# Optimization experiments

Measured on AMD Instinct MI355X. Metric: run time of the kernel, lower is better.

The kernel has to match this reference:

```python
import jax, jax.numpy as jnp
import numpy as np

B, T, E, H, V = 64, 256, 300, 512, 50000
G = 3 * H  # gates: r, z, n (PyTorch order)


def setup_inputs() -> dict:
    key = jax.random.key(0)
    ks = jax.random.split(key, 14)
    k = 1.0 / np.sqrt(H)
    u = lambda kk, sh: jax.random.uniform(kk, sh, jnp.float32, -k, k)
    x = jax.random.randint(ks[0], (B, T), 0, V)
    emb = jax.random.normal(ks[1], (V, E), jnp.float32) * 0.1
    emb = emb.at[0].set(0.0)  # padding_idx=0
    return {
        "x": x,
        "emb": emb,
        # layer 0: input E, both directions stacked on axis 0
        "w_ih0": u(ks[2], (2, G, E)),
        "w_hh0": u(ks[3], (2, G, H)),
        "b_ih0": u(ks[4], (2, G)),
        "b_hh0": u(ks[5], (2, G)),
        # layer 1: input 2H
        "w_ih1": u(ks[6], (2, G, 2 * H)),
        "w_hh1": u(ks[7], (2, G, 2 * H if False else H)) if False else u(ks[7], (2, G, H)),
        "b_ih1": u(ks[8], (2, G)),
        "b_hh1": u(ks[9], (2, G)),
        # classifier
        "w1": u(ks[10], (128, 2 * H)),
        "b1": u(ks[11], (128,)),
        "w2": u(ks[12], (2, 128)),
        "b2": u(ks[13], (2,)),
    }


def _gru_dir(x, w_ih, w_hh, b_ih, b_hh, reverse):
    # x: [B, T, in]; precompute input projections for all timesteps
    xp = jnp.einsum('bti,gi->btg', x, w_ih) + b_ih  # [B, T, 3H]

    def step(h, xp_t):
        gh = h @ w_hh.T + b_hh  # [B, 3H]
        r = jax.nn.sigmoid(xp_t[:, :H] + gh[:, :H])
        z = jax.nn.sigmoid(xp_t[:, H:2 * H] + gh[:, H:2 * H])
        n = jnp.tanh(xp_t[:, 2 * H:] + r * gh[:, 2 * H:])
        h = (1.0 - z) * n + z * h
        return h, h

    h0 = jnp.zeros((x.shape[0], H), x.dtype)
    _, ys = jax.lax.scan(step, h0, jnp.swapaxes(xp, 0, 1), reverse=reverse)
    return jnp.swapaxes(ys, 0, 1)  # [B, T, H], aligned to input positions


def _bigru_layer(x, w_ih, w_hh, b_ih, b_hh):
    f = _gru_dir(x, w_ih[0], w_hh[0], b_ih[0], b_hh[0], False)
    b = _gru_dir(x, w_ih[1], w_hh[1], b_ih[1], b_hh[1], True)
    return jnp.concatenate([f, b], axis=-1)  # [B, T, 2H]


def reference(x, emb, w_ih0, w_hh0, b_ih0, b_hh0, w_ih1, w_hh1, b_ih1, b_hh1, w1, b1, w2, b2):
    e = emb[x]  # [B, T, E]
    h = _bigru_layer(e, w_ih0, w_hh0, b_ih0, b_hh0)
    h = _bigru_layer(h, w_ih1, w_hh1, b_ih1, b_hh1)  # dropout=eval mode (identity)
    pooled = jnp.max(h, axis=1)  # [B, 2H]
    hid = jax.nn.relu(pooled @ w1.T + b1)
    return hid @ w2.T + b2  # [B, 2]
```

## Files before the change

kernel.cpp:

```cpp
#include <hip/hip_runtime.h>

#define BB 64
#define TLEN 256
#define HH 512
#define GG 1536
#define EPAD 320
#define NN 3072
#define MM 16384

typedef __attribute__((ext_vector_type(8))) __fp16 half8;
typedef __attribute__((ext_vector_type(4))) __fp16 half4;
typedef __attribute__((ext_vector_type(4))) float floatx4;

typedef union { unsigned long long u[2]; half8 v; } hpack;
typedef union { half4 h4; unsigned long long u; } hpack4;
typedef union { unsigned short s; __fp16 h; } hu16;

__global__ __launch_bounds__(256) void g2_prep(const int* __restrict__ x,
                                               const float* __restrict__ emb,
                                               __fp16* __restrict__ e,
                                               const float* __restrict__ w_ih0,
                                               __fp16* __restrict__ w0p,
                                               const float* __restrict__ w_ih1,
                                               __fp16* __restrict__ w1c) {
  const int blk = blockIdx.x;
  if (blk < 960) {
    int idx = blk * 256 + threadIdx.x;
    int row = idx / 80;
    int c = idx - row * 80;
    half4 v = {0, 0, 0, 0};
    if (c < 75) {
      float4 f = *(const float4*)&w_ih0[(long)row * 300 + c * 4];
      v[0] = (__fp16)f.x; v[1] = (__fp16)f.y; v[2] = (__fp16)f.z; v[3] = (__fp16)f.w;
    }
    *(half4*)&w0p[row * EPAD + c * 4] = v;
  } else if (blk < 2496) {
    long idx = (long)(blk - 960) * 256 + threadIdx.x;
    float4 a = *(const float4*)&w_ih1[idx * 8];
    float4 b = *(const float4*)&w_ih1[idx * 8 + 4];
    half8 o;
    o[0] = (__fp16)a.x; o[1] = (__fp16)a.y; o[2] = (__fp16)a.z; o[3] = (__fp16)a.w;
    o[4] = (__fp16)b.x; o[5] = (__fp16)b.y; o[6] = (__fp16)b.z; o[7] = (__fp16)b.w;
    *(half8*)&w1c[idx * 8] = o;
  } else {
    int idx = (blk - 2496) * 256 + threadIdx.x;
    int row = idx / 80;
    int c = idx - row * 80;
    int t = row >> 6, b = row & 63;
    half4 v = {0, 0, 0, 0};
    if (c < 75) {
      int xi = x[b * TLEN + t];
      float4 f = *(const float4*)&emb[(long)xi * 300 + c * 4];
      v[0] = (__fp16)f.x; v[1] = (__fp16)f.y; v[2] = (__fp16)f.z; v[3] = (__fp16)f.w;
    }
    *(half4*)&e[row * EPAD + c * 4] = v;
  }
}

__global__ __launch_bounds__(256, 1) void g2_fused(
    const float* __restrict__ whh,
    const float* __restrict__ bhh,
    __fp16* xp,
    __fp16* __restrict__ hout,
    __fp16* __restrict__ hx,
    const __fp16* __restrict__ ga,
    const __fp16* __restrict__ gw,
    const float* __restrict__ gbias,
    int Kp) {
  __shared__ __align__(16) char smem[65536];
  __shared__ __fp16 hst[4][16][20];
  const unsigned long long SENT = 0xFFFFFFFFFFFFFFFFULL;
  const int bid = blockIdx.x;
  const int tid = threadIdx.x;
  const int lane = tid & 63, wv = tid >> 6;
  const int nsub = lane & 15, quad = lane >> 4;

  if (bid >= 64) {
    const int gb = bid - 64;
    const int kb = gb / 24, nb = gb - kb * 24;
    const int mt = (kb & 1) ? (127 - (kb >> 1)) : (kb >> 1);
    const int m0 = mt << 7, n0 = nb << 7;
    __fp16 (*As)[72] = (__fp16(*)[72])smem;
    __fp16 (*Ws)[72] = (__fp16(*)[72])(smem + 18432);
    const int wm = (wv >> 1) << 6, wn = (wv & 1) << 6;
    floatx4 acc[4][4];
#pragma unroll
    for (int i = 0; i < 4; i++)
#pragma unroll
      for (int j = 0; j < 4; j++) acc[i][j] = (floatx4){0.f, 0.f, 0.f, 0.f};
    const int lr = tid >> 3;
    const int lc = (tid & 7) << 3;
    for (int ko = 0; ko < Kp; ko += 64) {
#pragma unroll
      for (int p = 0; p < 4; p++) {
        int r = lr + p * 32;
        *(half8*)&As[r][lc] = *(const half8*)&ga[(long)(m0 + r) * Kp + ko + lc];
        *(half8*)&Ws[r][lc] = *(const half8*)&gw[(long)(n0 + r) * Kp + ko + lc];
      }
      __syncthreads();
#pragma unroll
      for (int kk = 0; kk < 64; kk += 32) {
        half8 af[4], bf[4];
        const int kr = kk + (quad << 3);
#pragma unroll
        for (int i = 0; i < 4; i++) af[i] = *(const half8*)&As[wm + i * 16 + nsub][kr];
#pragma unroll
        for (int j = 0; j < 4; j++) bf[j] = *(const half8*)&Ws[wn + j * 16 + nsub][kr];
#pragma unroll
        for (int i = 0; i < 4; i++)
#pragma unroll
          for (int j = 0; j < 4; j++)
            acc[i][j] = __builtin_amdgcn_mfma_f32_16x16x32_f16(bf[j], af[i], acc[i][j], 0, 0, 0);
      }
      __syncthreads();
    }
#pragma unroll
    for (int i = 0; i < 4; i++) {
      const long row = m0 + wm + i * 16 + nsub;
#pragma unroll
      for (int j = 0; j < 4; j++) {
        const int col = n0 + wn + j * 16 + (quad << 2);
        const float* bvp = &gbias[col];
        hpack4 pk;
#pragma unroll
        for (int q = 0; q < 4; q++) pk.h4[q] = (__fp16)(acc[i][j][q] + bvp[q]);
        __hip_atomic_store((unsigned long long*)(xp + row * (long)NN + col), pk.u,
                           __ATOMIC_RELAXED, __HIP_MEMORY_SCOPE_AGENT);
      }
    }
    return;
  }

  const int gi = bid & 3;
  const int uo = bid >> 2;
  const int d = gi >> 1, g = gi & 1;
  const int U0 = uo << 5;
  const int mb = wv & 1, ut = wv >> 1;
  const int bq = (g << 5) + (mb << 4);
  const int ul = (ut << 4) + nsub;

  half8 wr_[16];
  {
    const float* wrbase = whh + ((long)d * GG + U0 + ul) * HH;
#pragma unroll
    for (int kk = 0; kk < 16; kk++) {
      const float* src = wrbase + (kk << 5) + (quad << 3);
      float4 a = *(const float4*)&src[0];
      float4 b = *(const float4*)&src[4];
      half8 o;
      o[0] = (__fp16)a.x; o[1] = (__fp16)a.y; o[2] = (__fp16)a.z; o[3] = (__fp16)a.w;
      o[4] = (__fp16)b.x; o[5] = (__fp16)b.y; o[6] = (__fp16)b.z; o[7] = (__fp16)b.w;
      wr_[kk] = o;
    }
  }
  half8 (*Wf)[16][64] = (half8(*)[16][64])smem;
  for (int e = tid; e < 4096; e += 256) {
    int lane_e = e & 63;
    int kk = (e >> 6) & 15;
    int utx = (e >> 10) & 1;
    int gate = (e >> 11) & 1;
    int unit = U0 + (utx << 4) + (lane_e & 15);
    int col = (kk << 5) + ((lane_e >> 4) << 3);
    const float* src = whh + ((long)d * GG + (gate + 1) * HH + unit) * HH + col;
    float4 a = *(const float4*)&src[0];
    float4 b = *(const float4*)&src[4];
    half8 o;
    o[0] = (__fp16)a.x; o[1] = (__fp16)a.y; o[2] = (__fp16)a.z; o[3] = (__fp16)a.w;
    o[4] = (__fp16)b.x; o[5] = (__fp16)b.y; o[6] = (__fp16)b.z; o[7] = (__fp16)b.w;
    Wf[gate * 2 + utx][kk][lane_e] = o;
  }
  __syncthreads();

  const float bhr = bhh[d * GG + U0 + ul];
  const float bhz = bhh[d * GG + HH + U0 + ul];
  const float bhn = bhh[d * GG + 2 * HH + U0 + ul];

  const int cidx = ((quad >> 1) << 6) + (nsub << 2) + ((quad & 1) << 1);
  const int pr = lane & 15, pc4 = (lane >> 4) << 2;
  const int pidx = (uo << 7) + (ut << 6) + (pr << 2) + (pc4 >> 2);
  const int sh = (nsub & 3) << 4;
  const long xoff = (long)(bq + (quad << 2)) * NN + d * GG + U0 + (ut << 4) + (nsub & 12);

  float hprev[4] = {0.f, 0.f, 0.f, 0.f};
  hpack4 xw[12];

  {
    const int tt0 = d ? (TLEN - 1) : 0;
    const __fp16* xb0 = xp + (long)(tt0 * BB) * NN + xoff;
#pragma unroll
    for (int i = 0; i < 4; i++) {
      const unsigned long long* q = (const unsigned long long*)(xb0 + (long)i * NN);
      xw[i * 3 + 0].u = __hip_atomic_load(&q[0], __ATOMIC_RELAXED, __HIP_MEMORY_SCOPE_AGENT);
      xw[i * 3 + 1].u = __hip_atomic_load(&q[HH / 4], __ATOMIC_RELAXED, __HIP_MEMORY_SCOPE_AGENT);
      xw[i * 3 + 2].u = __hip_atomic_load(&q[2 * HH / 4], __ATOMIC_RELAXED, __HIP_MEMORY_SCOPE_AGENT);
    }
  }

  for (int s = 0; s < TLEN; s++) {
    const int tt = d ? (TLEN - 1 - s) : s;
    const __fp16* xb0 = xp + (long)(tt * BB) * NN + xoff;
    const unsigned long long* hx8 = 0;
    hpack u[16];
    floatx4 ar0 = {0.f, 0.f, 0.f, 0.f}, ar1 = ar0, az0 = ar0, az1 = ar0, an0 = ar0, an1 = ar0;
    if (s > 0) {
      const int pt = d ? (tt + 1) : (tt - 1);
      hx8 = (const unsigned long long*)(hx + ((((long)pt * 2 + d) * 2 + g) * 2 + mb) * 8192);
#pragma unroll
      for (int kk = 0; kk < 16; kk++) {
        u[kk].u[0] = __hip_atomic_load(&hx8[kk * 128 + cidx], __ATOMIC_RELAXED, __HIP_MEMORY_SCOPE_AGENT);
        u[kk].u[1] = __hip_atomic_load(&hx8[kk * 128 + cidx + 1], __ATOMIC_RELAXED, __HIP_MEMORY_SCOPE_AGENT);
      }
#pragma unroll
      for (int g4 = 0; g4 < 4; g4++) {
        int bad = 0;
#pragma unroll
        for (int kk = g4 * 4; kk < g4 * 4 + 4; kk++)
          bad |= (u[kk].u[0] == SENT) | (u[kk].u[1] == SENT);
        while (__any(bad)) {
#pragma unroll
          for (int kk = g4 * 4; kk < g4 * 4 + 4; kk++) {
            u[kk].u[0] = __hip_atomic_load(&hx8[kk * 128 + cidx], __ATOMIC_RELAXED, __HIP_MEMORY_SCOPE_AGENT);
            u[kk].u[1] = __hip_atomic_load(&hx8[kk * 128 + cidx + 1], __ATOMIC_RELAXED, __HIP_MEMORY_SCOPE_AGENT);
          }
          bad = 0;
#pragma unroll
          for (int kk = g4 * 4; kk < g4 * 4 + 4; kk++)
            bad |= (u[kk].u[0] == SENT) | (u[kk].u[1] == SENT);
        }
#pragma unroll
        for (int kk = g4 * 4; kk < g4 * 4 + 4; kk += 2) {
          half8 wzA = Wf[ut][kk][lane],     wnA = Wf[2 + ut][kk][lane];
          half8 wzB = Wf[ut][kk + 1][lane], wnB = Wf[2 + ut][kk + 1][lane];
          ar0 = __builtin_amdgcn_mfma_f32_16x16x32_f16(u[kk].v, wr_[kk], ar0, 0, 0, 0);
          az0 = __builtin_amdgcn_mfma_f32_16x16x32_f16(u[kk].v, wzA, az0, 0, 0, 0);
          an0 = __builtin_amdgcn_mfma_f32_16x16x32_f16(u[kk].v, wnA, an0, 0, 0, 0);
          ar1 = __builtin_amdgcn_mfma_f32_16x16x32_f16(u[kk + 1].v, wr_[kk + 1], ar1, 0, 0, 0);
          az1 = __builtin_amdgcn_mfma_f32_16x16x32_f16(u[kk + 1].v, wzB, az1, 0, 0, 0);
          an1 = __builtin_amdgcn_mfma_f32_16x16x32_f16(u[kk + 1].v, wnB, an1, 0, 0, 0);
        }
      }
    }
    {
      int xbad = 0;
#pragma unroll
      for (int w = 0; w < 12; w++) xbad |= (xw[w].u == SENT);
      while (__any(xbad)) {
#pragma unroll
        for (int i = 0; i < 4; i++) {
          const unsigned long long* q = (const unsigned long long*)(xb0 + (long)i * NN);
          xw[i * 3 + 0].u = __hip_atomic_load(&q[0], __ATOMIC_RELAXED, __HIP_MEMORY_SCOPE_AGENT);
          xw[i * 3 + 1].u = __hip_atomic_load(&q[HH / 4], __ATOMIC_RELAXED, __HIP_MEMORY_SCOPE_AGENT);
          xw[i * 3 + 2].u = __hip_atomic_load(&q[2 * HH / 4], __ATOMIC_RELAXED, __HIP_MEMORY_SCOPE_AGENT);
        }
        xbad = 0;
#pragma unroll
        for (int w = 0; w < 12; w++) xbad |= (xw[w].u == SENT);
      }
    }
    float xr[4], xz[4], xn[4];
#pragma unroll
    for (int i = 0; i < 4; i++) {
      hu16 t0, t1, t2;
      t0.s = (unsigned short)(xw[i * 3 + 0].u >> sh);
      t1.s = (unsigned short)(xw[i * 3 + 1].u >> sh);
      t2.s = (unsigned short)(xw[i * 3 + 2].u >> sh);
      xr[i] = (float)t0.h; xz[i] = (float)t1.h; xn[i] = (float)t2.h;
    }
#pragma unroll
    for (int i = 0; i < 4; i++) {
      float grv = ar0[i] + ar1[i] + xr[i] + bhr;
      float gzv = az0[i] + az1[i] + xz[i] + bhz;
      float gnv = an0[i] + an1[i] + bhn;
      float rg = 1.f / (1.f + __expf(-grv));
      float zg = 1.f / (1.f + __expf(-gzv));
      float ex = __expf(2.f * (xn[i] + rg * gnv));
      float ng = 1.f - 2.f / (ex + 1.f);
      float hv = (1.f - zg) * ng + zg * hprev[i];
      hprev[i] = hv;
      hst[wv][(quad << 2) + i][nsub] = (__fp16)hv;
    }
    asm volatile("" ::: "memory");
    {
      hpack4 pk;
      pk.h4 = *(const half4*)&hst[wv][pr][pc4];
      unsigned long long* hxw =
          (unsigned long long*)(hx + ((((long)tt * 2 + d) * 2 + g) * 2 + mb) * 8192);
      __hip_atomic_store(&hxw[pidx], pk.u, __ATOMIC_RELAXED, __HIP_MEMORY_SCOPE_AGENT);
      if (hout)
        *(half4*)&hout[(long)(tt * BB + (g << 5) + (mb << 4) + pr) * 1024 +
                       d * HH + U0 + (ut << 4) + pc4] = pk.h4;
    }
    if (s + 1 < TLEN) {
      const int tn = d ? (tt - 1) : (tt + 1);
      const __fp16* xbn = xp + (long)(tn * BB) * NN + xoff;
#pragma unroll
      for (int i = 0; i < 4; i++) {
        const unsigned long long* q = (const unsigned long long*)(xbn + (long)i * NN);
        xw[i * 3 + 0].u = __hip_atomic_load(&q[0], __ATOMIC_RELAXED, __HIP_MEMORY_SCOPE_AGENT);
        xw[i * 3 + 1].u = __hip_atomic_load(&q[HH / 4], __ATOMIC_RELAXED, __HIP_MEMORY_SCOPE_AGENT);
        xw[i * 3 + 2].u = __hip_atomic_load(&q[2 * HH / 4], __ATOMIC_RELAXED, __HIP_MEMORY_SCOPE_AGENT);
      }
    }
  }
}

__global__ __launch_bounds__(256) void g2_poolhead(const __fp16* __restrict__ hx1,
                                                   const float* __restrict__ w1,
                                                   const float* __restrict__ b1,
                                                   const float* __restrict__ w2,
                                                   const float* __restrict__ b2,
                                                   float* __restrict__ out) {
  __shared__ float pl[1024];
  __shared__ float hid[128];
  const int b = blockIdx.x, tid = threadIdx.x;
  const int dd = tid >> 7;
  const int j0 = (tid & 127) << 2;
  const int gg = b >> 5, mbb = (b >> 4) & 1, prr = b & 15;
  const long ebase = ((long)(dd * 4 + gg * 2 + mbb)) * 8192 +
                     ((j0 >> 5) << 9) + (((j0 >> 4) & 1) << 8) + (prr << 4) + (j0 & 15);
  const __fp16* p = hx1 + ebase;
  float m[4] = {-3e38f, -3e38f, -3e38f, -3e38f};
  for (int t = 0; t < TLEN; t++) {
    half4 v = *(const half4*)(p + (long)t * 8 * 8192);
#pragma unroll
    for (int q = 0; q < 4; q++) m[q] = fmaxf(m[q], (float)v[q]);
  }
#pragma unroll
  for (int q = 0; q < 4; q++) pl[dd * 512 + j0 + q] = m[q];
  __syncthreads();
  if (tid < 128) {
    float acc = b1[tid];
    const float* wr = w1 + (long)tid * 1024;
    for (int k = 0; k < 1024; k += 4) {
      float4 w = *(const float4*)&wr[k];
      acc += pl[k] * w.x + pl[k + 1] * w.y + pl[k + 2] * w.z + pl[k + 3] * w.w;
    }
    hid[tid] = fmaxf(acc, 0.f);
  }
  __syncthreads();
  if (tid < 2) {
    float a = b2[tid];
    for (int k = 0; k < 128; k++) a += hid[k] * w2[tid * 128 + k];
    out[b * 2 + tid] = a;
  }
}

extern "C" void kernel_launch(void* const* d_in, const int* in_sizes, int n_in,
                              void* d_out, int out_size, void* d_ws, size_t ws_size,
                              hipStream_t stream) {
  (void)in_sizes; (void)n_in; (void)out_size; (void)ws_size;
  const int* x = (const int*)d_in[0];
  const float* emb = (const float*)d_in[1];
  const float* w_ih0 = (const float*)d_in[2];
  const float* w_hh0 = (const float*)d_in[3];
  const float* b_ih0 = (const float*)d_in[4];
  const float* b_hh0 = (const float*)d_in[5];
  const float* w_ih1 = (const float*)d_in[6];
  const float* w_hh1 = (const float*)d_in[7];
  const float* b_ih1 = (const float*)d_in[8];
  const float* b_hh1 = (const float*)d_in[9];
  const float* w1 = (const float*)d_in[10];
  const float* b1 = (const float*)d_in[11];
  const float* w2 = (const float*)d_in[12];
  const float* b2 = (const float*)d_in[13];

  char* ws = (char*)d_ws;
  __fp16* xp = (__fp16*)(ws + 0);
  __fp16* h0 = (__fp16*)(ws + 100663296);
  __fp16* h1 = (__fp16*)(ws + 134217728);
  __fp16* e_pad = (__fp16*)(ws + 167772160);
  __fp16* w0p = (__fp16*)(ws + 178257920);
  __fp16* w1c = (__fp16*)(ws + 180224000);

  (void)hipMemsetAsync(h1, 0xFF, 33554432, stream);
  (void)hipMemsetAsync(xp, 0xFF, 100663296, stream);
  g2_prep<<<7616, 256, 0, stream>>>(x, emb, e_pad, w_ih0, w0p, w_ih1, w1c);
  g2_fused<<<3136, 256, 0, stream>>>(w_hh0, b_hh0, xp, h0, h1, e_pad, w0p, b_ih0, EPAD);
  (void)hipMemsetAsync(h1, 0xFF, 33554432, stream);
  (void)hipMemsetAsync(xp, 0xFF, 100663296, stream);
  g2_fused<<<3136, 256, 0, stream>>>(w_hh1, b_hh1, xp, (__fp16*)0, h1, h0, w1c, b_ih1, 1024);
  g2_poolhead<<<64, 256, 0, stream>>>(h1, w1, b1, w2, b2, (float*)d_out);
}
```

Before: 1.963 ms.

## Fuse embedding gather and weight conversion into GEMM loads; pool inside recurrence

Drops the separate prep kernel. The GEMM tile loaders now gather embedding rows by token index and convert fp32 weights to fp16 on the fly, which removes the padded fp16 staging buffers and an extra launch. The layer-1 recurrent blocks keep a running max of each hidden output, so the head kernel reads a small pooled buffer instead of re-scanning the whole h1 sequence. The trade-off is repeated per-tile conversion work: each weight tile is converted many times across the M tiles, fp32 loads double the weight bytes read, and the layer-0 loader gains an irregular gather plus a boundary branch.

Result: slower. 2.159 ms (+10.0%).

```diff
diff --git a/kernel.cpp b/kernel.cpp
--- a/kernel.cpp
+++ b/kernel.cpp
@@ -16,47 +16,6 @@
 typedef union { half4 h4; unsigned long long u; } hpack4;
 typedef union { unsigned short s; __fp16 h; } hu16;
 
-__global__ __launch_bounds__(256) void g2_prep(const int* __restrict__ x,
-                                               const float* __restrict__ emb,
-                                               __fp16* __restrict__ e,
-                                               const float* __restrict__ w_ih0,
-                                               __fp16* __restrict__ w0p,
-                                               const float* __restrict__ w_ih1,
-                                               __fp16* __restrict__ w1c) {
-  const int blk = blockIdx.x;
-  if (blk < 960) {
-    int idx = blk * 256 + threadIdx.x;
-    int row = idx / 80;
-    int c = idx - row * 80;
-    half4 v = {0, 0, 0, 0};
-    if (c < 75) {
-      float4 f = *(const float4*)&w_ih0[(long)row * 300 + c * 4];
-      v[0] = (__fp16)f.x; v[1] = (__fp16)f.y; v[2] = (__fp16)f.z; v[3] = (__fp16)f.w;
-    }
-    *(half4*)&w0p[row * EPAD + c * 4] = v;
-  } else if (blk < 2496) {
-    long idx = (long)(blk - 960) * 256 + threadIdx.x;
-    float4 a = *(const float4*)&w_ih1[idx * 8];
-    float4 b = *(const float4*)&w_ih1[idx * 8 + 4];
-    half8 o;
-    o[0] = (__fp16)a.x; o[1] = (__fp16)a.y; o[2] = (__fp16)a.z; o[3] = (__fp16)a.w;
-    o[4] = (__fp16)b.x; o[5] = (__fp16)b.y; o[6] = (__fp16)b.z; o[7] = (__fp16)b.w;
-    *(half8*)&w1c[idx * 8] = o;
-  } else {
-    int idx = (blk - 2496) * 256 + threadIdx.x;
-    int row = idx / 80;
-    int c = idx - row * 80;
-    int t = row >> 6, b = row & 63;
-    half4 v = {0, 0, 0, 0};
-    if (c < 75) {
-      int xi = x[b * TLEN + t];
-      float4 f = *(const float4*)&emb[(long)xi * 300 + c * 4];
-      v[0] = (__fp16)f.x; v[1] = (__fp16)f.y; v[2] = (__fp16)f.z; v[3] = (__fp16)f.w;
-    }
-    *(half4*)&e[row * EPAD + c * 4] = v;
-  }
-}
-
 __global__ __launch_bounds__(256, 1) void g2_fused(
     const float* __restrict__ whh,
     const float* __restrict__ bhh,
@@ -64,9 +23,12 @@
     __fp16* __restrict__ hout,
     __fp16* __restrict__ hx,
     const __fp16* __restrict__ ga,
-    const __fp16* __restrict__ gw,
+    const float* __restrict__ gwf,
     const float* __restrict__ gbias,
-    int Kp) {
+    int Kp, int lay,
+    const int* __restrict__ gx,
+    const float* __restrict__ gemb,
+    float* __restrict__ pooled) {
   __shared__ __align__(16) char smem[65536];
   __shared__ __fp16 hst[4][16][20];
   const unsigned long long SENT = 0xFFFFFFFFFFFFFFFFULL;
@@ -91,11 +53,54 @@
     const int lr = tid >> 3;
     const int lc = (tid & 7) << 3;
     for (int ko = 0; ko < Kp; ko += 64) {
+      const int c0 = ko + lc;
 #pragma unroll
       for (int p = 0; p < 4; p++) {
         int r = lr + p * 32;
-        *(half8*)&As[r][lc] = *(const half8*)&ga[(long)(m0 + r) * Kp + ko + lc];
-        *(half8*)&Ws[r][lc] = *(const half8*)&gw[(long)(n0 + r) * Kp + ko + lc];
+        if (lay == 0) {
+          int row = m0 + r;
+          int t = row >> 6, b = row & 63;
+          int xi = gx[b * TLEN + t];
+          const float* er = gemb + (long)xi * 300;
+          half8 oa;
+          if (c0 + 8 <= 300) {
+            float4 a = *(const float4*)&er[c0];
+            float4 b2 = *(const float4*)&er[c0 + 4];
+            oa[0] = (__fp16)a.x; oa[1] = (__fp16)a.y; oa[2] = (__fp16)a.z; oa[3] = (__fp16)a.w;
+            oa[4] = (__fp16)b2.x; oa[5] = (__fp16)b2.y; oa[6] = (__fp16)b2.z; oa[7] = (__fp16)b2.w;
+          } else {
+#pragma unroll
+            for (int q = 0; q < 8; q++) {
+              int c = c0 + q;
+              oa[q] = (c < 300) ? (__fp16)er[c] : (__fp16)0.f;
+            }
+          }
+          *(half8*)&As[r][lc] = oa;
+          const float* wr2 = gwf + (long)(n0 + r) * 300;
+          half8 ow;
+          if (c0 + 8 <= 300) {
+            float4 a = *(const float4*)&wr2[c0];
+            float4 b2 = *(const float4*)&wr2[c0 + 4];
+            ow[0] = (__fp16)a.x; ow[1] = (__fp16)a.y; ow[2] = (__fp16)a.z; ow[3] = (__fp16)a.w;
+            ow[4] = (__fp16)b2.x; ow[5] = (__fp16)b2.y; ow[6] = (__fp16)b2.z; ow[7] = (__fp16)b2.w;
+          } else {
+#pragma unroll
+            for (int q = 0; q < 8; q++) {
+              int c = c0 + q;
+              ow[q] = (c < 300) ? (__fp16)wr2[c] : (__fp16)0.f;
+            }
+          }
+          *(half8*)&Ws[r][lc] = ow;
+        } else {
+          *(half8*)&As[r][lc] = *(const half8*)&ga[(long)(m0 + r) * Kp + c0];
+          const float* wr2 = gwf + (long)(n0 + r) * 1024;
+          float4 a = *(const float4*)&wr2[c0];
+          float4 b2 = *(const float4*)&wr2[c0 + 4];
+          half8 ow;
+          ow[0] = (__fp16)a.x; ow[1] = (__fp16)a.y; ow[2] = (__fp16)a.z; ow[3] = (__fp16)a.w;
+          ow[4] = (__fp16)b2.x; ow[5] = (__fp16)b2.y; ow[6] = (__fp16)b2.z; ow[7] = (__fp16)b2.w;
+          *(half8*)&Ws[r][lc] = ow;
+        }
       }
       __syncthreads();
 #pragma unroll
@@ -182,6 +187,7 @@
   const long xoff = (long)(bq + (quad << 2)) * NN + d * GG + U0 + (ut << 4) + (nsub & 12);
 
   float hprev[4] = {0.f, 0.f, 0.f, 0.f};
+  float pmax[4] = {-3e38f, -3e38f, -3e38f, -3e38f};
   hpack4 xw[12];
 
   {
@@ -289,6 +295,10 @@
       if (hout)
         *(half4*)&hout[(long)(tt * BB + (g << 5) + (mb << 4) + pr) * 1024 +
                        d * HH + U0 + (ut << 4) + pc4] = pk.h4;
+      if (pooled) {
+#pragma unroll
+        for (int i = 0; i < 4; i++) pmax[i] = fmaxf(pmax[i], (float)pk.h4[i]);
+      }
     }
     if (s + 1 < TLEN) {
       const int tn = d ? (tt - 1) : (tt + 1);
@@ -302,46 +312,36 @@
       }
     }
   }
+  if (pooled) {
+    float4 o = {pmax[0], pmax[1], pmax[2], pmax[3]};
+    *(float4*)&pooled[(long)((g << 5) + (mb << 4) + pr) * 1024 +
+                      d * HH + U0 + (ut << 4) + pc4] = o;
+  }
 }
 
-__global__ __launch_bounds__(256) void g2_poolhead(const __fp16* __restrict__ hx1,
-                                                   const float* __restrict__ w1,
-                                                   const float* __restrict__ b1,
-                                                   const float* __restrict__ w2,
-                                                   const float* __restrict__ b2,
-                                                   float* __restrict__ out) {
+__global__ __launch_bounds__(128) void g2_head(const float* __restrict__ pooled,
+                                               const float* __restrict__ w1,
+                                               const float* __restrict__ b1,
+                                               const float* __restrict__ w2,
+                                               const float* __restrict__ b2,
+                                               float* __restrict__ out) {
   __shared__ float pl[1024];
   __shared__ float hid[128];
-  const int b = blockIdx.x, tid = threadIdx.x;
-  const int dd = tid >> 7;
-  const int j0 = (tid & 127) << 2;
-  const int gg = b >> 5, mbb = (b >> 4) & 1, prr = b & 15;
-  const long ebase = ((long)(dd * 4 + gg * 2 + mbb)) * 8192 +
-                     ((j0 >> 5) << 9) + (((j0 >> 4) & 1) << 8) + (prr << 4) + (j0 & 15);
-  const __fp16* p = hx1 + ebase;
-  float m[4] = {-3e38f, -3e38f, -3e38f, -3e38f};
-  for (int t = 0; t < TLEN; t++) {
-    half4 v = *(const half4*)(p + (long)t * 8 * 8192);
-#pragma unroll
-    for (int q = 0; q < 4; q++) m[q] = fmaxf(m[q], (float)v[q]);
-  }
-#pragma unroll
-  for (int q = 0; q < 4; q++) pl[dd * 512 + j0 + q] = m[q];
+  int b = blockIdx.x, j = threadIdx.x;
+  for (int k = j; k < 1024; k += 128) pl[k] = pooled[b * 1024 + k];
   __syncthreads();
-  if (tid < 128) {
-    float acc = b1[tid];
-    const float* wr = w1 + (long)tid * 1024;
-    for (int k = 0; k < 1024; k += 4) {
-      float4 w = *(const float4*)&wr[k];
-      acc += pl[k] * w.x + pl[k + 1] * w.y + pl[k + 2] * w.z + pl[k + 3] * w.w;
-    }
-    hid[tid] = fmaxf(acc, 0.f);
-  }
+  float acc = b1[j];
+  const float* wr = w1 + (long)j * 1024;
+  for (int k = 0; k < 1024; k += 4) {
+    float4 w = *(const float4*)&wr[k];
+    acc += pl[k] * w.x + pl[k + 1] * w.y + pl[k + 2] * w.z + pl[k + 3] * w.w;
+  }
+  hid[j] = fmaxf(acc, 0.f);
   __syncthreads();
-  if (tid < 2) {
-    float a = b2[tid];
-    for (int k = 0; k < 128; k++) a += hid[k] * w2[tid * 128 + k];
-    out[b * 2 + tid] = a;
+  if (j < 2) {
+    float a = b2[j];
+    for (int k = 0; k < 128; k++) a += hid[k] * w2[j * 128 + k];
+    out[b * 2 + j] = a;
   }
 }
 
@@ -368,16 +368,17 @@
   __fp16* xp = (__fp16*)(ws + 0);
   __fp16* h0 = (__fp16*)(ws + 100663296);
   __fp16* h1 = (__fp16*)(ws + 134217728);
-  __fp16* e_pad = (__fp16*)(ws + 167772160);
-  __fp16* w0p = (__fp16*)(ws + 178257920);
-  __fp16* w1c = (__fp16*)(ws + 180224000);
+  float* pooled = (float*)(ws + 167772160);
 
   (void)hipMemsetAsync(h1, 0xFF, 33554432, stream);
   (void)hipMemsetAsync(xp, 0xFF, 100663296, stream);
-  g2_prep<<<7616, 256, 0, stream>>>(x, emb, e_pad, w_ih0, w0p, w_ih1, w1c);
-  g2_fused<<<3136, 256, 0, stream>>>(w_hh0, b_hh0, xp, h0, h1, e_pad, w0p, b_ih0, EPAD);
+  g2_fused<<<3136, 256, 0, stream>>>(w_hh0, b_hh0, xp, h0, h1,
+                                     (const __fp16*)0, w_ih0, b_ih0, EPAD, 0,
+                                     x, emb, (float*)0);
   (void)hipMemsetAsync(h1, 0xFF, 33554432, stream);
   (void)hipMemsetAsync(xp, 0xFF, 100663296, stream);
-  g2_fused<<<3136, 256, 0, stream>>>(w_hh1, b_hh1, xp, (__fp16*)0, h1, h0, w1c, b_ih1, 1024);
-  g2_poolhead<<<64, 256, 0, stream>>>(h1, w1, b1, w2, b2, (float*)d_out);
+  g2_fused<<<3136, 256, 0, stream>>>(w_hh1, b_hh1, xp, (__fp16*)0, h1,
+                                     h0, w_ih1, b_ih1, 1024, 1,
+                                     (const int*)0, (const float*)0, pooled);
+  g2_head<<<64, 128, 0, stream>>>(pooled, w1, b1, w2, b2, (float*)d_out);
 }
```
